# Kernel optimization log

Hardware: AMD Instinct MI355X
Metric: run time of the kernel (lower is better)

The kernel has to match this reference:

```python
import jax, jax.numpy as jnp
import numpy as np

EMBED_DIM = 2048
N_HEADS = 32
N_GROUPS = 8
HEAD_SIZE = EMBED_DIM // N_HEADS  # 64
SCALE = HEAD_SIZE ** -0.5
B, S = 2, 2048


def setup_inputs() -> dict:
    key = jax.random.key(0)
    ks = jax.random.split(key, 7)
    kv_dim = N_GROUPS * HEAD_SIZE
    x = jax.random.normal(ks[0], (B, S, EMBED_DIM), dtype=jnp.float32)
    # Linear weights stored [in, out] (y = x @ W), matching torch nn.Linear math.
    Wq = jax.random.normal(ks[1], (EMBED_DIM, EMBED_DIM), dtype=jnp.float32) * (EMBED_DIM ** -0.5)
    Wk = jax.random.normal(ks[2], (EMBED_DIM, kv_dim), dtype=jnp.float32) * (EMBED_DIM ** -0.5)
    Wv = jax.random.normal(ks[3], (EMBED_DIM, kv_dim), dtype=jnp.float32) * (EMBED_DIM ** -0.5)
    Wo = jax.random.normal(ks[4], (EMBED_DIM, EMBED_DIM), dtype=jnp.float32) * (EMBED_DIM ** -0.5)
    bo = jnp.zeros((EMBED_DIM,), dtype=jnp.float32)
    # causal boolean mask [S, S], broadcast over batch and heads
    mask = jnp.tril(jnp.ones((S, S), dtype=jnp.bool_))
    return {"x": x, "Wq": Wq, "Wk": Wk, "Wv": Wv, "Wo": Wo, "bo": bo, "mask": mask}


def reference(x, Wq, Wk, Wv, Wo, bo, mask):
    B_, S_, E = x.shape
    q = (x @ Wq).reshape(B_, S_, N_HEADS, HEAD_SIZE).transpose(0, 2, 1, 3)   # [B,H,S,D]
    k = (x @ Wk).reshape(B_, S_, N_GROUPS, HEAD_SIZE).transpose(0, 2, 1, 3)  # [B,G,S,D]
    v = (x @ Wv).reshape(B_, S_, N_GROUPS, HEAD_SIZE).transpose(0, 2, 1, 3)
    # GQA: each KV head serves H//G consecutive query heads (matches torch expand+reshape)
    rep = N_HEADS // N_GROUPS
    k = jnp.repeat(k, rep, axis=1)  # [B,H,S,D]
    v = jnp.repeat(v, rep, axis=1)
    scores = SCALE * jnp.einsum("bhqd,bhkd->bhqk", q, k)          # [B,H,S,S]
    scores = jnp.where(mask, scores, -jnp.inf)
    weights = jax.nn.softmax(scores, axis=-1)                      # dropout in eval mode (identity)
    attn = jnp.einsum("bhqk,bhkd->bhqd", weights, v)               # [B,H,S,D]
    attn = attn.transpose(0, 2, 1, 3).reshape(B_, S_, E)
    return attn @ Wo + bo
```

## Files before the change

### kernel.cpp

```cpp
#include <hip/hip_runtime.h>
#include <hip/hip_fp16.h>

#define E_DIM 2048
#define S_LEN 2048
#define NH 32
#define HD 64
#define KV_DIM 512
#define QKV_N 3072
#define M_ROWS 4096
#define QK_SCALE 0.18033688011112042f

typedef __bf16 bf16x8 __attribute__((ext_vector_type(8)));
typedef float f32x4 __attribute__((ext_vector_type(4)));

__device__ __forceinline__ void async_lds16(const __bf16* g, __bf16* l) {
    __builtin_amdgcn_global_load_lds(
        (const __attribute__((address_space(1))) void*)g,
        (__attribute__((address_space(3))) void*)l, 16, 0, 0);
}

#define BAR() asm volatile("s_barrier" ::: "memory")

__global__ void k_convert(const float* __restrict__ x, __bf16* __restrict__ xb, int n) {
    int i = (blockIdx.x * blockDim.x + threadIdx.x) * 4;
    if (i < n) {
        float4 v = *(const float4*)(x + i);
        xb[i + 0] = (__bf16)v.x;
        xb[i + 1] = (__bf16)v.y;
        xb[i + 2] = (__bf16)v.z;
        xb[i + 3] = (__bf16)v.w;
    }
}

__global__ void k_transpose_all(const float* __restrict__ Wq, const float* __restrict__ Wk,
                                const float* __restrict__ Wv, const float* __restrict__ Wo,
                                __bf16* __restrict__ WtAll, __bf16* __restrict__ WoT) {
    const int which = blockIdx.z;
    const float* W;
    __bf16* dst;
    int N;
    float scale = 1.f;
    if (which == 0)      { W = Wq; dst = WtAll;                                    N = E_DIM;  scale = QK_SCALE; }
    else if (which == 1) { W = Wk; dst = WtAll + (size_t)E_DIM * E_DIM;            N = KV_DIM; }
    else if (which == 2) { W = Wv; dst = WtAll + (size_t)(E_DIM + KV_DIM) * E_DIM; N = KV_DIM; }
    else                 { W = Wo; dst = WoT;                                      N = E_DIM;  }
    const int n0 = blockIdx.x * 32;
    if (n0 >= N) return;
    const int k0 = blockIdx.y * 32;
    __shared__ float tile[32][33];
    int tx = threadIdx.x, ty = threadIdx.y;
#pragma unroll
    for (int j = 0; j < 4; ++j)
        tile[ty + j * 8][tx] = W[(size_t)(k0 + ty + j * 8) * N + n0 + tx];
    __syncthreads();
#pragma unroll
    for (int j = 0; j < 4; ++j)
        dst[(size_t)(n0 + ty + j * 8) * E_DIM + k0 + tx] = (__bf16)(tile[tx][ty + j * 8] * scale);
}

#define STG(g, l, bb, hh, kt) do {                                                              \
    async_lds16((g) + (size_t)((hh) * 128) * K + (size_t)(kt) * 64,                             \
                (l) + (bb) * 16384 + (hh) * 8192);                                              \
    async_lds16((g) + (size_t)((hh) * 128 + 64) * K + (size_t)(kt) * 64,                        \
                (l) + (bb) * 16384 + (hh) * 8192 + 4096);                                       \
} while (0)

#define LDA_(p, mq) do {                                                                        \
    _Pragma("unroll") for (int i_ = 0; i_ < 4; ++i_) {                                          \
        const char* rp_ = pAs + (p) * 32768 + ((mq) * 128 + rA + i_ * 16) * 128;                \
        a[i_][0] = *(const bf16x8*)(rp_ + swzk0);                                               \
        a[i_][1] = *(const bf16x8*)(rp_ + swzk1);                                               \
    }                                                                                           \
} while (0)

#define LDB_(p, nq, b) do {                                                                     \
    _Pragma("unroll") for (int j_ = 0; j_ < 2; ++j_) {                                          \
        const char* rp_ = pBs + (p) * 32768 + ((nq) * 128 + rB + j_ * 16) * 128;                \
        b[j_][0] = *(const bf16x8*)(rp_ + swzk0);                                               \
        b[j_][1] = *(const bf16x8*)(rp_ + swzk1);                                               \
    }                                                                                           \
} while (0)

#define MM(mq, nq, b) do {                                                                      \
    __builtin_amdgcn_s_setprio(1);                                                              \
    _Pragma("unroll") for (int i_ = 0; i_ < 4; ++i_)                                            \
    _Pragma("unroll") for (int j_ = 0; j_ < 2; ++j_) {                                          \
        acc[mq][nq][i_][j_] = __builtin_amdgcn_mfma_f32_16x16x32_bf16(                          \
            a[i_][0], b[j_][0], acc[mq][nq][i_][j_], 0, 0, 0);                                  \
        acc[mq][nq][i_][j_] = __builtin_amdgcn_mfma_f32_16x16x32_bf16(                          \
            a[i_][1], b[j_][1], acc[mq][nq][i_][j_], 0, 0, 0);                                  \
    }                                                                                           \
    __builtin_amdgcn_s_setprio(0);                                                              \
} while (0)

#define GROUP(p, kt, S1, S2, WAITSTMT) do {                                                     \
    LDA_(p, 0);                                                                                 \
    LDB_(p, 0, b0);                                                                             \
    if (S1) STG(gA, lA, (p) ^ 1, 1, (kt) + 1);                                                  \
    BAR(); MM(0, 0, b0); BAR();                                                                 \
    LDB_(p, 1, b1);                                                                             \
    if (S2) STG(gA, lA, (p), 0, (kt) + 2);                                                      \
    BAR(); MM(0, 1, b1); BAR();                                                                 \
    LDA_(p, 1);                                                                                 \
    if (S2) STG(gB, lB, (p), 0, (kt) + 2);                                                      \
    BAR(); MM(1, 1, b1); BAR();                                                                 \
    if (S2) STG(gB, lB, (p), 1, (kt) + 2);                                                      \
    WAITSTMT;                                                                                   \
    BAR(); MM(1, 0, b0); BAR();                                                                 \
} while (0)

__global__ __launch_bounds__(512, 2)
void k_gemm8(const __bf16* __restrict__ A, const __bf16* __restrict__ Bt,
             __bf16* __restrict__ C, int M, int N, int K) {
    __shared__ __attribute__((aligned(16))) __bf16 As[2][16384];
    __shared__ __attribute__((aligned(16))) __bf16 Bs[2][16384];
    const int T = K >> 6;
    const int nbx = N >> 8;
    const int bid = blockIdx.x;
    const int swz = (bid & 7) * ((int)gridDim.x >> 3) + (bid >> 3);
    const int m0 = (swz / nbx) << 8;
    const int n0 = (swz % nbx) << 8;

    const int t = threadIdx.x;
    const int lane = t & 63, w = t >> 6;
    const int quad = lane >> 4, l16 = lane & 15;
    const int wr = w >> 2, wc = w & 3;

    const int rbase = w * 8 + (lane >> 3);
    const int cswz = ((lane & 7) ^ (lane >> 3)) * 8;
    const __bf16* gA = A + (size_t)(m0 + rbase) * K + cswz;
    const __bf16* gB = Bt + (size_t)(n0 + rbase) * K + cswz;
    __bf16* lA = &As[0][0] + w * 512;
    __bf16* lB = &Bs[0][0] + w * 512;

    const int swzk0 = ((0 + quad) ^ (l16 & 7)) * 16;
    const int swzk1 = ((4 + quad) ^ (l16 & 7)) * 16;
    const int rA = wr * 64 + l16;
    const int rB = wc * 32 + l16;
    const char* pAs = (const char*)&As[0][0];
    const char* pBs = (const char*)&Bs[0][0];

    f32x4 acc[2][2][4][2] = {};
    bf16x8 a[4][2], b0[2][2], b1[2][2];

    STG(gA, lA, 0, 0, 0); STG(gA, lA, 0, 1, 0);
    STG(gB, lB, 0, 0, 0); STG(gB, lB, 0, 1, 0);
    STG(gA, lA, 1, 0, 1);
    STG(gB, lB, 1, 0, 1); STG(gB, lB, 1, 1, 1);
    asm volatile("s_waitcnt vmcnt(6)" ::: "memory");
    BAR();

    int p = 0;
    for (int kt = 0; kt < T - 2; ++kt) {
        GROUP(p, kt, 1, 1, asm volatile("s_waitcnt vmcnt(6)" ::: "memory"));
        p ^= 1;
    }
    GROUP(p, T - 2, 1, 0, asm volatile("s_waitcnt vmcnt(0)" ::: "memory"));
    p ^= 1;
    GROUP(p, T - 1, 0, 0, (void)0);

#pragma unroll
    for (int mq = 0; mq < 2; ++mq)
#pragma unroll
        for (int nq = 0; nq < 2; ++nq)
#pragma unroll
            for (int i = 0; i < 4; ++i)
#pragma unroll
                for (int j = 0; j < 2; ++j) {
                    const int row = m0 + mq * 128 + wr * 64 + i * 16 + quad * 4;
                    const int col = n0 + nq * 128 + wc * 32 + j * 16 + l16;
#pragma unroll
                    for (int r = 0; r < 4; ++r)
                        C[(size_t)(row + r) * N + col] = (__bf16)acc[mq][nq][i][j][r];
                }
    (void)M;
}

template <int OUT_F32>
__global__ __launch_bounds__(256, 2)
void k_gemm_bt(const __bf16* __restrict__ A, const __bf16* __restrict__ Bt,
               void* __restrict__ Cout, const float* __restrict__ bias,
               int M, int N, int K) {
    __shared__ __attribute__((aligned(16))) __bf16 As2[128 * 64];
    __shared__ __attribute__((aligned(16))) __bf16 Bs2[128 * 64];
    const int t = threadIdx.x;
    const int lane = t & 63, wave = t >> 6;
    const int quad = lane >> 4, l16 = lane & 15;
    const int wr = wave >> 1, wc = wave & 1;
    const int m0 = blockIdx.y * 128, n0 = blockIdx.x * 128;

    const int srow = t >> 2;
    const int sblk = (t & 3) ^ ((t >> 3) & 3);
    const __bf16* gA0 = A + (size_t)(m0 + srow) * K + sblk * 8;
    const __bf16* gA1 = gA0 + (size_t)64 * K;
    const __bf16* gB0 = Bt + (size_t)(n0 + srow) * K + sblk * 8;
    const __bf16* gB1 = gB0 + (size_t)64 * K;

    f32x4 acc[4][4] = {};

    for (int k0 = 0; k0 < K; k0 += 64) {
#pragma unroll
        for (int ks = 0; ks < 2; ++ks) {
            async_lds16(gA0 + k0 + ks * 32, As2 + ks * 4096 + wave * 512);
            async_lds16(gA1 + k0 + ks * 32, As2 + ks * 4096 + 2048 + wave * 512);
            async_lds16(gB0 + k0 + ks * 32, Bs2 + ks * 4096 + wave * 512);
            async_lds16(gB1 + k0 + ks * 32, Bs2 + ks * 4096 + 2048 + wave * 512);
        }
        __syncthreads();
#pragma unroll
        for (int ks = 0; ks < 2; ++ks) {
            bf16x8 af[4], bfr[4];
#pragma unroll
            for (int i = 0; i < 4; ++i) {
                const int row = wr * 64 + i * 16 + l16;
                af[i] = *(const bf16x8*)((const char*)As2 + ks * 8192 + row * 64 +
                                         ((quad ^ ((row >> 1) & 3)) * 16));
            }
#pragma unroll
            for (int j = 0; j < 4; ++j) {
                const int row = wc * 64 + j * 16 + l16;
                bfr[j] = *(const bf16x8*)((const char*)Bs2 + ks * 8192 + row * 64 +
                                          ((quad ^ ((row >> 1) & 3)) * 16));
            }
#pragma unroll
            for (int i = 0; i < 4; ++i)
#pragma unroll
                for (int j = 0; j < 4; ++j)
                    acc[i][j] = __builtin_amdgcn_mfma_f32_16x16x32_bf16(af[i], bfr[j], acc[i][j], 0, 0, 0);
        }
        __syncthreads();
    }

#pragma unroll
    for (int i = 0; i < 4; ++i)
#pragma unroll
        for (int j = 0; j < 4; ++j) {
            const int row = m0 + wr * 64 + i * 16 + quad * 4;
            const int col = n0 + wc * 64 + j * 16 + l16;
#pragma unroll
            for (int r = 0; r < 4; ++r) {
                float v = acc[i][j][r];
                if (OUT_F32) ((float*)Cout)[(size_t)(row + r) * N + col] = v + bias[col];
                else ((__bf16*)Cout)[(size_t)(row + r) * N + col] = (__bf16)v;
            }
        }
}

#define MICRO(kb, mm, qs) do {                                                                  \
    const int qsub0_ = q0 + (qs) * 64;                                                          \
    const int qrow_ = qsub0_ + qr16;                                                            \
    const bool diag_ = ((kb) == qsub0_);                                                        \
    f32x4 sA_[4], sB_[4];                                                                       \
    __builtin_amdgcn_s_setprio(1);                                                              \
    _Pragma("unroll") for (int kt_ = 0; kt_ < 4; ++kt_) {                                       \
        const int kr_ = (mm) * 64 + kt_ * 16 + l16;                                             \
        const char* kb__ = (const char*)Kls + kr_ * 128;                                        \
        bf16x8 kf0_ = *(const bf16x8*)(kb__ + ((quad ^ (kr_ & 7)) * 16));                       \
        bf16x8 kf1_ = *(const bf16x8*)(kb__ + (((4 + quad) ^ (kr_ & 7)) * 16));                 \
        f32x4 z_ = {};                                                                          \
        z_ = __builtin_amdgcn_mfma_f32_16x16x32_bf16(kf0_, qf[qs][0][0], z_, 0, 0, 0);          \
        sA_[kt_] = __builtin_amdgcn_mfma_f32_16x16x32_bf16(kf1_, qf[qs][0][1], z_, 0, 0, 0);    \
        f32x4 w_ = {};                                                                          \
        w_ = __builtin_amdgcn_mfma_f32_16x16x32_bf16(kf0_, qf[qs][1][0], w_, 0, 0, 0);          \
        sB_[kt_] = __builtin_amdgcn_mfma_f32_16x16x32_bf16(kf1_, qf[qs][1][1], w_, 0, 0, 0);    \
    }                                                                                           \
    __builtin_amdgcn_s_setprio(0);                                                              \
    _Pragma("unroll") for (int hf_ = 0; hf_ < 2; ++hf_) {                                       \
        bf16x8 vf_[4];                                                                          \
        const int koff_ = (mm) * 64 + hf_ * 32;                                                 \
        _Pragma("unroll") for (int cc_ = 0; cc_ < 4; ++cc_)                                     \
            vf_[cc_] = *(const bf16x8*)&vT[cc_ * 16 + l16][koff_ + quad * 8];                   \
        _Pragma("unroll") for (int h_ = 0; h_ < 2; ++h_) {                                      \
            char* prow_ = (char*)&pT[wave][h_][0] + l16 * 64;                                   \
            float lsum_ = 0.f;                                                                  \
            _Pragma("unroll") for (int u_ = 0; u_ < 2; ++u_) {                                  \
                const int kt_ = 2 * hf_ + u_;                                                   \
                f32x4 pv_;                                                                      \
                _Pragma("unroll") for (int r_ = 0; r_ < 4; ++r_)                                \
                    pv_[r_] = exp2f(h_ ? sB_[kt_][r_] : sA_[kt_][r_]);                          \
                if (diag_) {                                                                    \
                    const int kbase_ = (kb) + kt_ * 16 + quad * 4;                              \
                    _Pragma("unroll") for (int r_ = 0; r_ < 4; ++r_)                            \
                        if (kbase_ + r_ > qrow_) pv_[r_] = 0.f;                                 \
                }                                                                               \
                _Pragma("unroll") for (int r_ = 0; r_ < 4; ++r_) lsum_ += pv_[r_];              \
                __bf16 pb_[4];                                                                  \
                _Pragma("unroll") for (int r_ = 0; r_ < 4; ++r_) pb_[r_] = (__bf16)pv_[r_];     \
                const int bi_ = (2 * u_ + (quad >> 1)) ^ pswz;                                  \
                *(uint2*)(prow_ + bi_ * 16 + (quad & 1) * 8) = *(const uint2*)pb_;              \
            }                                                                                   \
            l_st[qs][h_] += lsum_;                                                              \
            bf16x8 pf_ = *(const bf16x8*)(prow_ + ((quad ^ pswz) * 16));                        \
            __builtin_amdgcn_s_setprio(1);                                                      \
            _Pragma("unroll") for (int cc_ = 0; cc_ < 4; ++cc_)                                 \
                o[qs][h_][cc_] = __builtin_amdgcn_mfma_f32_16x16x32_bf16(                       \
                    vf_[cc_], pf_, o[qs][h_][cc_], 0, 0, 0);                                    \
            __builtin_amdgcn_s_setprio(0);                                                      \
        }                                                                                       \
    }                                                                                           \
} while (0)

__global__ __launch_bounds__(256, 2)
void k_attn(const __bf16* __restrict__ qkv, __half* __restrict__ partO,
            float* __restrict__ partL) {
    const int xr = (int)(gridDim.x - 1 - blockIdx.x);
    int qi, c;
    if (xr < 4)       { qi = xr;                   c = 0; }
    else if (xr < 12) { qi = 4 + ((xr - 4) >> 1);  c = (xr - 4) & 1; }
    else if (xr < 24) { qi = 8 + (xr - 12) / 3;    c = (xr - 12) % 3; }
    else              { qi = 12 + ((xr - 24) >> 2); c = (xr - 24) & 3; }
    const int q0 = qi * 128;
    const int k_lo = c * 512;
    const int k_hi = min(k_lo + 512, q0 + 128);

    const int gp = blockIdx.y;
    const int g = gp >> 1;
    const int h0 = g * 4 + (gp & 1) * 2;
    const int b = blockIdx.z;
    const int t = threadIdx.x;
    const int lane = t & 63, wave = t >> 6;
    const int quad = lane >> 4, l16 = lane & 15;

    __shared__ __attribute__((aligned(16))) __bf16 Kls[128 * 64];
    __shared__ __attribute__((aligned(16))) __bf16 vT[64][136];
    __shared__ __attribute__((aligned(16))) __bf16 pT[4][2][512];

    const __bf16* base = qkv + (size_t)b * S_LEN * QKV_N;
    const int qr16 = wave * 16 + l16;

    bf16x8 qf[2][2][2];
#pragma unroll
    for (int qs = 0; qs < 2; ++qs)
#pragma unroll
        for (int h = 0; h < 2; ++h)
#pragma unroll
            for (int s = 0; s < 2; ++s)
                qf[qs][h][s] = *(const bf16x8*)(base + (size_t)(q0 + qs * 64 + qr16) * QKV_N +
                                                (h0 + h) * HD + s * 32 + quad * 8);

    f32x4 o[2][2][4] = {};
    float l_st[2][2] = {};

    const int vkey = lane * 2, vdg = wave * 16;
    const __bf16* vsrc = base + (E_DIM + KV_DIM) + g * HD + vdg;
    const __bf16* ksrc = base + E_DIM + g * HD;

    const int klocal = lane >> 3;
    const int kdblk = (lane & 7) ^ (klocal & 7);
    const __bf16* gk_base = ksrc + (size_t)(wave * 32 + klocal) * QKV_N + kdblk * 8;
    __bf16* lk_base = Kls + wave * 2048;

    const int pswz = (l16 >> 1) & 3;

    for (int kv0 = k_lo; kv0 < k_hi; kv0 += 128) {
#pragma unroll
        for (int i = 0; i < 4; ++i)
            async_lds16(gk_base + (size_t)(kv0 + i * 8) * QKV_N, lk_base + i * 512);

        const __bf16* vp = vsrc + (size_t)(kv0 + vkey) * QKV_N;
        uint4 va0 = *(const uint4*)(vp);
        uint4 va1 = *(const uint4*)(vp + 8);
        uint4 vb0 = *(const uint4*)(vp + QKV_N);
        uint4 vb1 = *(const uint4*)(vp + QKV_N + 8);

        {
            const unsigned short* a0 = (const unsigned short*)&va0;
            const unsigned short* a1 = (const unsigned short*)&va1;
            const unsigned short* b0_ = (const unsigned short*)&vb0;
            const unsigned short* b1_ = (const unsigned short*)&vb1;
#pragma unroll
            for (int j = 0; j < 8; ++j) {
                *(uint32_t*)&vT[vdg + j][vkey] = (uint32_t)a0[j] | ((uint32_t)b0_[j] << 16);
                *(uint32_t*)&vT[vdg + 8 + j][vkey] = (uint32_t)a1[j] | ((uint32_t)b1_[j] << 16);
            }
        }
        __syncthreads();

        MICRO(kv0, 0, 0);
        if (kv0 < q0)
            MICRO(kv0 + 64, 1, 0);
        MICRO(kv0, 0, 1);
        if (kv0 < q0 + 64)
            MICRO(kv0 + 64, 1, 1);

        __syncthreads();
    }

    const size_t blk = ((size_t)b * 16 + gp) * 40 + xr;
    const size_t pb = blk * (size_t)(2 * 128 * 64);
#pragma unroll
    for (int qs = 0; qs < 2; ++qs)
#pragma unroll
        for (int h = 0; h < 2; ++h) {
            float lt = l_st[qs][h];
            lt += __shfl_xor(lt, 16);
            lt += __shfl_xor(lt, 32);
            const float inv = 1.f / lt;
            __half* prowO = partO + pb + (size_t)(h * 128 + qs * 64 + qr16) * 64 + quad * 4;
#pragma unroll
            for (int dt = 0; dt < 4; ++dt) {
                __half ob[4];
#pragma unroll
                for (int r = 0; r < 4; ++r) ob[r] = __float2half(o[qs][h][dt][r] * inv);
                *(uint2*)(prowO + dt * 16) = *(const uint2*)ob;
            }
            if (quad == 0)
                partL[blk * 256 + h * 128 + qs * 64 + qr16] = lt;
        }
}

__global__ __launch_bounds__(256, 4)
void k_combine(const __half* __restrict__ partO, const float* __restrict__ partL,
               __bf16* __restrict__ attnb) {
    const int qh = blockIdx.x, gp = blockIdx.y, b = blockIdx.z;
    const int qi = qh >> 1, h = qh & 1;
    const int nc = (qi >> 2) + 1;
    int x0;
    if (qi < 4) x0 = qi;
    else if (qi < 8) x0 = 4 + (qi - 4) * 2;
    else if (qi < 12) x0 = 12 + (qi - 8) * 3;
    else x0 = 24 + (qi - 12) * 4;

    const int t = threadIdx.x;
    const int row = t >> 1, half = t & 1;
    const int d0 = half * 32;
    const size_t gbase = ((size_t)b * 16 + gp) * 40;

    float W = 0.f;
    float acc[32];
#pragma unroll
    for (int i = 0; i < 32; ++i) acc[i] = 0.f;
    for (int cc = 0; cc < nc; ++cc) {
        const float a = partL[(gbase + x0 + cc) * 256 + h * 128 + row];
        W += a;
        const __half* src = partO + (gbase + x0 + cc) * (size_t)(2 * 128 * 64) +
                            (size_t)(h * 128 + row) * 64 + d0;
#pragma unroll
        for (int i = 0; i < 32; i += 8) {
            uint4 u = *(const uint4*)(src + i);
            const __half* hs = (const __half*)&u;
#pragma unroll
            for (int j = 0; j < 8; ++j) acc[i + j] += a * __half2float(hs[j]);
        }
    }
    const float inv = 1.f / W;
    const int h_abs = (gp >> 1) * 4 + (gp & 1) * 2 + h;
    __bf16* dst = attnb + ((size_t)b * S_LEN + qi * 128 + row) * E_DIM + h_abs * 64 + d0;
#pragma unroll
    for (int i = 0; i < 32; i += 8) {
        __bf16 ob[8];
#pragma unroll
        for (int j = 0; j < 8; ++j) ob[j] = (__bf16)(acc[i + j] * inv);
        *(uint4*)(dst + i) = *(const uint4*)ob;
    }
}

extern "C" void kernel_launch(void* const* d_in, const int* in_sizes, int n_in,
                              void* d_out, int out_size, void* d_ws, size_t ws_size,
                              hipStream_t stream) {
    const float* x  = (const float*)d_in[0];
    const float* Wq = (const float*)d_in[1];
    const float* Wk = (const float*)d_in[2];
    const float* Wv = (const float*)d_in[3];
    const float* Wo = (const float*)d_in[4];
    const float* bo = (const float*)d_in[5];

    __bf16* xb    = (__bf16*)d_ws;
    __bf16* WtAll = xb + (size_t)M_ROWS * E_DIM;
    __bf16* WoT   = WtAll + (size_t)QKV_N * E_DIM;
    __bf16* qkv   = WoT + (size_t)E_DIM * E_DIM;
    __bf16* attnb = qkv + (size_t)M_ROWS * QKV_N;
    __half* partO = (__half*)(attnb + (size_t)M_ROWS * E_DIM);
    float* partL  = (float*)(partO + (size_t)1280 * 2 * 128 * 64);

    k_convert<<<(M_ROWS * E_DIM / 4 + 255) / 256, 256, 0, stream>>>(x, xb, M_ROWS * E_DIM);
    k_transpose_all<<<dim3(64, 64, 4), dim3(32, 8), 0, stream>>>(Wq, Wk, Wv, Wo, WtAll, WoT);

    k_gemm8<<<dim3((M_ROWS / 256) * (QKV_N / 256)), 512, 0, stream>>>(
        xb, WtAll, qkv, M_ROWS, QKV_N, E_DIM);

    k_attn<<<dim3(40, 16, 2), 256, 0, stream>>>(qkv, partO, partL);
    k_combine<<<dim3(32, 16, 2), 256, 0, stream>>>(partO, partL, attnb);

    k_gemm_bt<1><<<dim3(E_DIM / 128, M_ROWS / 128), 256, 0, stream>>>(
        attnb, WoT, d_out, bo, M_ROWS, E_DIM, E_DIM);
}
```

Measured before the change: 328.7 us.

## Feed P to PV MFMA directly from registers via 16x16x16 instructions

Removes the per-wave LDS round trip that reshuffled the softmax probabilities into the B-operand layout of the 16x16x32 MFMA. The PV product now uses the 16x16x16 bf16 MFMA, whose operand layout matches the QK^T output fragment, so P stays in registers and the pT shared buffer goes away. In exchange it issues twice as many MFMAs at half the K depth, uses inline asm with an s_nop that the compiler cannot schedule around, and drops the setprio hints.

```diff
diff --git a/kernel.cpp b/kernel.cpp
--- a/kernel.cpp
+++ b/kernel.cpp
@@ -11,12 +11,19 @@
 #define QK_SCALE 0.18033688011112042f
 
 typedef __bf16 bf16x8 __attribute__((ext_vector_type(8)));
+typedef __bf16 bf16x4 __attribute__((ext_vector_type(4)));
 typedef float f32x4 __attribute__((ext_vector_type(4)));
 
 __device__ __forceinline__ void async_lds16(const __bf16* g, __bf16* l) {
     __builtin_amdgcn_global_load_lds(
         (const __attribute__((address_space(1))) void*)g,
         (__attribute__((address_space(3))) void*)l, 16, 0, 0);
+}
+
+__device__ __forceinline__ f32x4 mfma16(bf16x4 a, bf16x4 b, f32x4 c) {
+    asm("s_nop 1\n\tv_mfma_f32_16x16x16_bf16 %0, %1, %2, %0"
+        : "+v"(c) : "v"(a), "v"(b));
+    return c;
 }
 
 #define BAR() asm volatile("s_barrier" ::: "memory")
@@ -265,37 +272,25 @@
         sB_[kt_] = __builtin_amdgcn_mfma_f32_16x16x32_bf16(kf1_, qf[qs][1][1], w_, 0, 0, 0);    \
     }                                                                                           \
     __builtin_amdgcn_s_setprio(0);                                                              \
-    _Pragma("unroll") for (int hf_ = 0; hf_ < 2; ++hf_) {                                       \
-        bf16x8 vf_[4];                                                                          \
-        const int koff_ = (mm) * 64 + hf_ * 32;                                                 \
+    _Pragma("unroll") for (int kt_ = 0; kt_ < 4; ++kt_) {                                       \
+        bf16x4 v4_[4];                                                                          \
+        const int koff_ = (mm) * 64 + kt_ * 16 + quad * 4;                                      \
         _Pragma("unroll") for (int cc_ = 0; cc_ < 4; ++cc_)                                     \
-            vf_[cc_] = *(const bf16x8*)&vT[cc_ * 16 + l16][koff_ + quad * 8];                   \
+            v4_[cc_] = *(const bf16x4*)&vT[cc_ * 16 + l16][koff_];                              \
         _Pragma("unroll") for (int h_ = 0; h_ < 2; ++h_) {                                      \
-            char* prow_ = (char*)&pT[wave][h_][0] + l16 * 64;                                   \
-            float lsum_ = 0.f;                                                                  \
-            _Pragma("unroll") for (int u_ = 0; u_ < 2; ++u_) {                                  \
-                const int kt_ = 2 * hf_ + u_;                                                   \
-                f32x4 pv_;                                                                      \
+            f32x4 sc_ = h_ ? sB_[kt_] : sA_[kt_];                                               \
+            f32x4 p_;                                                                           \
+            _Pragma("unroll") for (int r_ = 0; r_ < 4; ++r_) p_[r_] = exp2f(sc_[r_]);           \
+            if (diag_) {                                                                        \
+                const int kbase_ = (kb) + kt_ * 16 + quad * 4;                                  \
                 _Pragma("unroll") for (int r_ = 0; r_ < 4; ++r_)                                \
-                    pv_[r_] = exp2f(h_ ? sB_[kt_][r_] : sA_[kt_][r_]);                          \
-                if (diag_) {                                                                    \
-                    const int kbase_ = (kb) + kt_ * 16 + quad * 4;                              \
-                    _Pragma("unroll") for (int r_ = 0; r_ < 4; ++r_)                            \
-                        if (kbase_ + r_ > qrow_) pv_[r_] = 0.f;                                 \
-                }                                                                               \
-                _Pragma("unroll") for (int r_ = 0; r_ < 4; ++r_) lsum_ += pv_[r_];              \
-                __bf16 pb_[4];                                                                  \
-                _Pragma("unroll") for (int r_ = 0; r_ < 4; ++r_) pb_[r_] = (__bf16)pv_[r_];     \
-                const int bi_ = (2 * u_ + (quad >> 1)) ^ pswz;                                  \
-                *(uint2*)(prow_ + bi_ * 16 + (quad & 1) * 8) = *(const uint2*)pb_;              \
+                    if (kbase_ + r_ > qrow_) p_[r_] = 0.f;                                      \
             }                                                                                   \
-            l_st[qs][h_] += lsum_;                                                              \
-            bf16x8 pf_ = *(const bf16x8*)(prow_ + ((quad ^ pswz) * 16));                        \
-            __builtin_amdgcn_s_setprio(1);                                                      \
+            l_st[qs][h_] += p_[0] + p_[1] + p_[2] + p_[3];                                      \
+            bf16x4 pb_;                                                                         \
+            _Pragma("unroll") for (int r_ = 0; r_ < 4; ++r_) pb_[r_] = (__bf16)p_[r_];          \
             _Pragma("unroll") for (int cc_ = 0; cc_ < 4; ++cc_)                                 \
-                o[qs][h_][cc_] = __builtin_amdgcn_mfma_f32_16x16x32_bf16(                       \
-                    vf_[cc_], pf_, o[qs][h_][cc_], 0, 0, 0);                                    \
-            __builtin_amdgcn_s_setprio(0);                                                      \
+                o[qs][h_][cc_] = mfma16(v4_[cc_], pb_, o[qs][h_][cc_]);                         \
         }                                                                                       \
     }                                                                                           \
 } while (0)
@@ -323,7 +318,6 @@
 
     __shared__ __attribute__((aligned(16))) __bf16 Kls[128 * 64];
     __shared__ __attribute__((aligned(16))) __bf16 vT[64][136];
-    __shared__ __attribute__((aligned(16))) __bf16 pT[4][2][512];
 
     const __bf16* base = qkv + (size_t)b * S_LEN * QKV_N;
     const int qr16 = wave * 16 + l16;
@@ -349,8 +343,6 @@
     const int kdblk = (lane & 7) ^ (klocal & 7);
     const __bf16* gk_base = ksrc + (size_t)(wave * 32 + klocal) * QKV_N + kdblk * 8;
     __bf16* lk_base = Kls + wave * 2048;
-
-    const int pswz = (l16 >> 1) & 3;
 
     for (int kv0 = k_lo; kv0 < k_hi; kv0 += 128) {
 #pragma unroll
```

New measurement: 327.4 us. About the same (-0.4%).
